# Kernel optimization log

Hardware: AMD Instinct MI355X
Metric: run time of the kernel (lower is better)

## Reference

```python
import jax, jax.numpy as jnp
import numpy as np

NUM_FEATURES = 602
NUM_CLASSES = 41
HIDDEN = 8
HEADS1 = 8
HEADS2 = 1
N_NODES = 100000
N_EDGES = 1600000
NEG_SLOPE = 0.2  # PyG GATConv default leaky_relu slope
EPS = 1e-16      # PyG softmax denominator epsilon


def gat_conv(x, edge_index, W, att_src, att_dst, bias, heads, out_ch, concat):
    """Faithful PyG GATConv forward (eval mode, dropout disabled).
    x: [N, F_in], edge_index: [2, E] with row0=src, row1=dst.
    W: [F_in, heads*out_ch], att_src/att_dst: [heads, out_ch], bias: [heads*out_ch] or [out_ch].
    """
    N = x.shape[0]
    h = (x @ W).reshape(N, heads, out_ch)              # [N, H, C]
    a_src = jnp.einsum('nhc,hc->nh', h, att_src)       # [N, H]
    a_dst = jnp.einsum('nhc,hc->nh', h, att_dst)       # [N, H]
    src, dst = edge_index[0], edge_index[1]
    e = jax.nn.leaky_relu(a_src[src] + a_dst[dst], NEG_SLOPE)  # [E, H]
    # segment softmax over incoming edges of each dst node
    m = jax.ops.segment_max(e, dst, num_segments=N)    # [N, H]
    e = jnp.exp(e - m[dst])
    denom = jax.ops.segment_sum(e, dst, num_segments=N)  # [N, H]
    alpha = e / (denom[dst] + EPS)                     # [E, H]
    msg = h[src] * alpha[:, :, None]                   # [E, H, C]
    out = jax.ops.segment_sum(msg, dst, num_segments=N)  # [N, H, C]
    if concat:
        out = out.reshape(N, heads * out_ch)
    else:
        out = out.mean(axis=1)
    return out + bias


def setup_inputs() -> dict:
    key = jax.random.key(0)
    ks = jax.random.split(key, 10)
    x = jax.random.normal(ks[0], (N_NODES, NUM_FEATURES), dtype=jnp.float32)
    edge_index = jax.random.randint(ks[1], (2, N_EDGES), 0, N_NODES, dtype=jnp.int64)
    s = 0.1
    W1 = jax.random.normal(ks[2], (NUM_FEATURES, HEADS1 * HIDDEN), dtype=jnp.float32) * s
    att_src1 = jax.random.normal(ks[3], (HEADS1, HIDDEN), dtype=jnp.float32) * s
    att_dst1 = jax.random.normal(ks[4], (HEADS1, HIDDEN), dtype=jnp.float32) * s
    b1 = jnp.zeros((HEADS1 * HIDDEN,), dtype=jnp.float32)
    W2 = jax.random.normal(ks[5], (HEADS1 * HIDDEN, HEADS2 * NUM_CLASSES), dtype=jnp.float32) * s
    att_src2 = jax.random.normal(ks[6], (HEADS2, NUM_CLASSES), dtype=jnp.float32) * s
    att_dst2 = jax.random.normal(ks[7], (HEADS2, NUM_CLASSES), dtype=jnp.float32) * s
    b2 = jnp.zeros((NUM_CLASSES,), dtype=jnp.float32)
    return {"x": x, "edge_index": edge_index, "W1": W1, "att_src1": att_src1,
            "att_dst1": att_dst1, "b1": b1, "W2": W2, "att_src2": att_src2,
            "att_dst2": att_dst2, "b2": b2}


def reference(x, edge_index, W1, att_src1, att_dst1, b1, W2, att_src2, att_dst2, b2):
    # eval mode: all F.dropout calls are identity
    h = gat_conv(x, edge_index, W1, att_src1, att_dst1, b1, HEADS1, HIDDEN, concat=True)
    h = jax.nn.elu(h)
    h = gat_conv(h, edge_index, W2, att_src2, att_dst2, b2, HEADS2, NUM_CLASSES, concat=False)
    return jax.nn.log_softmax(h, axis=1)
```

## Files before the change

kernel.cpp:

```cpp
#include <hip/hip_runtime.h>
#include <math.h>

#define NN 100000
#define NE 1600000
#define F_IN 602
#define H1 8
#define C1 8
#define F_MID 64
#define NC 41
#define H2_LD 48
#define NEG_SLOPE 0.2f
#define WT_LD 640

#define LRELU(x) fmaxf((x), NEG_SLOPE * (x))

typedef __attribute__((ext_vector_type(8))) short short8;
typedef __attribute__((ext_vector_type(4))) float f32x4;

__device__ inline unsigned short f2bf(float f) {
    unsigned u = __builtin_bit_cast(unsigned, f);
    unsigned r = (u + 0x7FFFu + ((u >> 16) & 1u)) >> 16;
    return (unsigned short)r;
}

__global__ void zero_kernel(int4* __restrict__ p, int n4)
{
    int i = blockIdx.x * blockDim.x + threadIdx.x;
    if (i < n4) p[i] = make_int4(0, 0, 0, 0);
}

__global__ void prep_wt_kernel(const float* __restrict__ W, unsigned short* __restrict__ Wt)
{
    int idx = blockIdx.x * blockDim.x + threadIdx.x;
    if (idx >= F_MID * WT_LD) return;
    int col = idx / WT_LD, k = idx % WT_LD;
    Wt[idx] = (k < F_IN) ? f2bf(W[k * F_MID + col]) : (unsigned short)0;
}

__global__ __launch_bounds__(256) void gemm1_mfma(
    const float* __restrict__ x, const unsigned short* __restrict__ Wt,
    float* __restrict__ h, int N)
{
    __shared__ unsigned short As[64][40];
    __shared__ unsigned short Bs[64][40];

    int t = threadIdx.x;
    int lane = t & 63;
    int w = t >> 6;
    int l16 = lane & 15, lg = lane >> 4;
    int n0 = blockIdx.x * 64;

    int arow = t >> 2, aseg = t & 3;
    int grow = n0 + arow;
    const float* xrow = x + (size_t)(grow < N ? grow : 0) * F_IN + aseg * 8;
    int bcol = t >> 2;
    const unsigned short* wrow = Wt + (size_t)bcol * WT_LD + aseg * 8;

    f32x4 acc[4] = {};
    float2 av[4];
    uint4  bv;

    #pragma unroll
    for (int i = 0; i < 4; ++i) av[i] = *(const float2*)(xrow + i * 2);
    bv = *(const uint4*)(wrow);

    for (int kt = 0; kt < 19; ++kt) {
        __syncthreads();
        {
            unsigned short tmp[8];
            #pragma unroll
            for (int i = 0; i < 4; ++i) {
                tmp[i * 2]     = f2bf(av[i].x);
                tmp[i * 2 + 1] = f2bf(av[i].y);
            }
            *(uint4*)(&As[arow][aseg * 8]) = *(uint4*)tmp;
            *(uint4*)(&Bs[bcol][aseg * 8]) = bv;
        }
        __syncthreads();

        if (kt < 18) {
            int k0 = (kt + 1) * 32;
            if (kt + 1 < 18) {
                #pragma unroll
                for (int i = 0; i < 4; ++i) av[i] = *(const float2*)(xrow + k0 + i * 2);
            } else {
                #pragma unroll
                for (int i = 0; i < 4; ++i) {
                    int k = k0 + aseg * 8 + i * 2;
                    float a = (k < F_IN)     ? xrow[k0 + i * 2]     : 0.f;
                    float b = (k + 1 < F_IN) ? xrow[k0 + i * 2 + 1] : 0.f;
                    av[i] = make_float2(a, b);
                }
            }
            bv = *(const uint4*)(wrow + k0);
        }

        short8 afrag = *(const short8*)(&As[w * 16 + l16][lg * 8]);
        short8 bfrag[4];
        #pragma unroll
        for (int n = 0; n < 4; ++n)
            bfrag[n] = *(const short8*)(&Bs[n * 16 + l16][lg * 8]);
        #pragma unroll
        for (int n = 0; n < 4; ++n)
            acc[n] = __builtin_amdgcn_mfma_f32_16x16x32_bf16(afrag, bfrag[n], acc[n], 0, 0, 0);
    }

    #pragma unroll
    for (int r = 0; r < 4; ++r) {
        int row = n0 + w * 16 + lg * 4 + r;
        if (row < N) {
            #pragma unroll
            for (int n = 0; n < 4; ++n)
                h[(size_t)row * F_MID + n * 16 + l16] = acc[n][r];
        }
    }
}

__global__ void attn1_kernel(const float* __restrict__ h,
                             const float* __restrict__ attS,
                             const float* __restrict__ attD,
                             float* __restrict__ asrc, float* __restrict__ adst, int N)
{
    int idx = blockIdx.x * blockDim.x + threadIdx.x;
    if (idx >= N * H1) return;
    int n = idx >> 3, hh = idx & 7;
    float s = 0.f, d = 0.f;
    #pragma unroll
    for (int c = 0; c < C1; ++c) {
        float v = h[n * F_MID + hh * C1 + c];
        s += v * attS[hh * C1 + c];
        d += v * attD[hh * C1 + c];
    }
    asrc[idx] = s;
    adst[idx] = d;
}

__global__ void deg_kernel(const int* __restrict__ dst, int* __restrict__ deg, int E)
{
    int e = blockIdx.x * blockDim.x + threadIdx.x;
    if (e < E) atomicAdd(&deg[dst[e]], 1);
}

__global__ void scan1_kernel(const int* __restrict__ deg, int* __restrict__ bsum, int N)
{
    int b = blockIdx.x, t = threadIdx.x;
    int base = b * 1024 + t * 16;
    int s = 0;
    #pragma unroll
    for (int i = 0; i < 16; ++i) { int idx = base + i; if (idx < N) s += deg[idx]; }
    #pragma unroll
    for (int o = 32; o > 0; o >>= 1) s += __shfl_down(s, o);
    if (t == 0) bsum[b] = s;
}

__global__ void scan2_kernel(const int* __restrict__ bsum, int* __restrict__ boff,
                             int nb, int* __restrict__ offs, int N, int E)
{
    __shared__ int buf[128];
    int t = threadIdx.x;
    int v = (t < nb) ? bsum[t] : 0;
    buf[t] = v;
    __syncthreads();
    for (int o = 1; o < 128; o <<= 1) {
        int u = (t >= o) ? buf[t - o] : 0;
        __syncthreads();
        buf[t] += u;
        __syncthreads();
    }
    if (t < nb) boff[t] = buf[t] - v;
    if (t == 0) offs[N] = E;
}

__global__ void scan3_kernel(const int* __restrict__ deg, const int* __restrict__ boff,
                             int* __restrict__ offs, int N)
{
    int b = blockIdx.x, t = threadIdx.x;
    int base = b * 1024 + t * 16;
    int loc[16];
    int s = 0;
    #pragma unroll
    for (int i = 0; i < 16; ++i) {
        int idx = base + i;
        loc[i] = (idx < N) ? deg[idx] : 0;
        s += loc[i];
    }
    int inc = s;
    #pragma unroll
    for (int o = 1; o < 64; o <<= 1) {
        int u = __shfl_up(inc, o);
        if (t >= o) inc += u;
    }
    int run = inc - s + boff[b];
    #pragma unroll
    for (int i = 0; i < 16; ++i) {
        int idx = base + i;
        if (idx < N) offs[idx] = run;
        run += loc[i];
    }
}

__global__ void scatter_kernel(const int* __restrict__ src, const int* __restrict__ dst,
                               const int* __restrict__ offs, int* __restrict__ cursor,
                               int* __restrict__ srcs, int E)
{
    int e = blockIdx.x * blockDim.x + threadIdx.x;
    if (e < E) {
        int d = dst[e];
        int pos = offs[d] + atomicAdd(&cursor[d], 1);
        srcs[pos] = src[e];
    }
}

__global__ void agg1_kernel(const int* __restrict__ offs, const int* __restrict__ srcs,
                            const float* __restrict__ h1,
                            const float* __restrict__ asrc, const float* __restrict__ adst,
                            const float* __restrict__ b1,
                            float* __restrict__ out1, int N)
{
    int wave = (blockIdx.x * blockDim.x + threadIdx.x) >> 6;
    int lane = threadIdx.x & 63;
    if (wave >= N) return;
    int n = wave;
    int hh = lane >> 3;
    int beg = offs[n], end = offs[n + 1];
    float ad = adst[n * H1 + hh];

    float m = -INFINITY, den = 0.f, acc = 0.f;
    int i = beg;
    for (; i + 8 <= end; i += 8) {
        int s[8];
        #pragma unroll
        for (int j = 0; j < 8; ++j) s[j] = srcs[i + j];
        float a[8], v[8];
        #pragma unroll
        for (int j = 0; j < 8; ++j) a[j] = asrc[s[j] * H1 + hh];
        #pragma unroll
        for (int j = 0; j < 8; ++j) v[j] = h1[s[j] * F_MID + lane];
        float e[8];
        #pragma unroll
        for (int j = 0; j < 8; ++j) e[j] = LRELU(a[j] + ad);
        float m8 = fmaxf(fmaxf(fmaxf(e[0], e[1]), fmaxf(e[2], e[3])),
                         fmaxf(fmaxf(e[4], e[5]), fmaxf(e[6], e[7])));
        float mn = fmaxf(m, m8);
        float sc = __expf(m - mn);
        float p[8];
        #pragma unroll
        for (int j = 0; j < 8; ++j) p[j] = __expf(e[j] - mn);
        den = den * sc + (((p[0] + p[1]) + (p[2] + p[3])) + ((p[4] + p[5]) + (p[6] + p[7])));
        acc = acc * sc + (((p[0] * v[0] + p[1] * v[1]) + (p[2] * v[2] + p[3] * v[3]))
                        + ((p[4] * v[4] + p[5] * v[5]) + (p[6] * v[6] + p[7] * v[7])));
        m = mn;
    }
    for (; i < end; ++i) {
        int s = srcs[i];
        float e = LRELU(asrc[s * H1 + hh] + ad);
        float hv = h1[s * F_MID + lane];
        float mn = fmaxf(m, e);
        float sc = __expf(m - mn);
        float p  = __expf(e - mn);
        den = den * sc + p;
        acc = acc * sc + p * hv;
        m = mn;
    }
    float inv = 1.f / (den + 1e-16f);
    float v = acc * inv + b1[lane];
    out1[n * F_MID + lane] = v > 0.f ? v : expm1f(v);
}

__global__ __launch_bounds__(256) void gemm2_kernel(
    const float* __restrict__ out1, const float* __restrict__ W2,
    float* __restrict__ h2p, int N)
{
    __shared__ float ws[F_MID * NC];
    for (int i = threadIdx.x; i < F_MID * NC; i += 256) ws[i] = W2[i];
    __syncthreads();
    int idx = blockIdx.x * blockDim.x + threadIdx.x;
    if (idx >= N * NC) return;
    int n = idx / NC, j = idx % NC;
    const float* row = out1 + n * F_MID;
    float acc = 0.f;
    #pragma unroll
    for (int k = 0; k < F_MID; ++k) acc += row[k] * ws[k * NC + j];
    h2p[n * H2_LD + j] = acc;
}

__global__ void attn2_kernel(float* __restrict__ h2p,
                             const float* __restrict__ attS,
                             const float* __restrict__ attD,
                             float* __restrict__ adst, int N)
{
    int n = blockIdx.x * blockDim.x + threadIdx.x;
    if (n >= N) return;
    float s = 0.f, d = 0.f;
    #pragma unroll
    for (int j = 0; j < NC; ++j) {
        float v = h2p[n * H2_LD + j];
        s += v * attS[j];
        d += v * attD[j];
    }
    h2p[n * H2_LD + NC] = s;
    adst[n] = d;
}

__global__ void agg2_kernel(const int* __restrict__ offs, const int* __restrict__ srcs,
                            const float* __restrict__ h2p,
                            const float* __restrict__ adst,
                            const float* __restrict__ b2,
                            float* __restrict__ out, int N)
{
    int wave = (blockIdx.x * blockDim.x + threadIdx.x) >> 6;
    int lane = threadIdx.x & 63;
    if (wave >= N) return;
    int n = wave;
    int beg = offs[n], end = offs[n + 1];
    float ad = adst[n];
    bool act = lane < NC;
    int li = act ? lane : NC;

    float m = -INFINITY, den = 0.f, acc = 0.f;
    int i = beg;
    for (; i + 8 <= end; i += 8) {
        int s[8];
        #pragma unroll
        for (int j = 0; j < 8; ++j) s[j] = srcs[i + j];
        float hv[8];
        #pragma unroll
        for (int j = 0; j < 8; ++j) hv[j] = h2p[s[j] * H2_LD + li];
        float a[8];
        #pragma unroll
        for (int j = 0; j < 8; ++j) a[j] = __shfl(hv[j], NC);
        float e[8];
        #pragma unroll
        for (int j = 0; j < 8; ++j) e[j] = LRELU(a[j] + ad);
        float m8 = fmaxf(fmaxf(fmaxf(e[0], e[1]), fmaxf(e[2], e[3])),
                         fmaxf(fmaxf(e[4], e[5]), fmaxf(e[6], e[7])));
        float mn = fmaxf(m, m8);
        float sc = __expf(m - mn);
        float p[8];
        #pragma unroll
        for (int j = 0; j < 8; ++j) p[j] = __expf(e[j] - mn);
        den = den * sc + (((p[0] + p[1]) + (p[2] + p[3])) + ((p[4] + p[5]) + (p[6] + p[7])));
        acc = acc * sc + (((p[0] * hv[0] + p[1] * hv[1]) + (p[2] * hv[2] + p[3] * hv[3]))
                        + ((p[4] * hv[4] + p[5] * hv[5]) + (p[6] * hv[6] + p[7] * hv[7])));
        m = mn;
    }
    for (; i < end; ++i) {
        int s = srcs[i];
        float hv = h2p[s * H2_LD + li];
        float a = __shfl(hv, NC);
        float e = LRELU(a + ad);
        float mn = fmaxf(m, e);
        float sc = __expf(m - mn);
        float p  = __expf(e - mn);
        den = den * sc + p;
        acc = acc * sc + p * hv;
        m = mn;
    }
    float inv = 1.f / (den + 1e-16f);
    float v = act ? acc * inv + b2[lane] : -INFINITY;
    float mm = v;
    #pragma unroll
    for (int o = 32; o > 0; o >>= 1) mm = fmaxf(mm, __shfl_xor(mm, o));
    float ex = act ? __expf(v - mm) : 0.f;
    float S = ex;
    #pragma unroll
    for (int o = 32; o > 0; o >>= 1) S += __shfl_xor(S, o);
    if (act) out[n * NC + lane] = v - mm - logf(S);
}

extern "C" void kernel_launch(void* const* d_in, const int* in_sizes, int n_in,
                              void* d_out, int out_size, void* d_ws, size_t ws_size,
                              hipStream_t stream)
{
    const float* x     = (const float*)d_in[0];
    const int*   ei    = (const int*)  d_in[1];
    const float* W1    = (const float*)d_in[2];
    const float* attS1 = (const float*)d_in[3];
    const float* attD1 = (const float*)d_in[4];
    const float* b1    = (const float*)d_in[5];
    const float* W2    = (const float*)d_in[6];
    const float* attS2 = (const float*)d_in[7];
    const float* attD2 = (const float*)d_in[8];
    const float* b2    = (const float*)d_in[9];
    float* out = (float*)d_out;

    const int N = NN, E = NE;
    const int* src = ei;
    const int* dst = ei + E;

    char* p = (char*)d_ws;
    auto alloc = [&](size_t bytes) { char* r = p; p += (bytes + 255) & ~255ull; return r; };
    float* h1    = (float*)alloc((size_t)N * F_MID * 4);
    float* asrc1 = (float*)alloc((size_t)N * H1 * 4);
    float* adst1 = (float*)alloc((size_t)N * H1 * 4);
    float* out1  = (float*)alloc((size_t)N * F_MID * 4);
    float* h2p   = (float*)alloc((size_t)N * H2_LD * 4);
    float* adst2 = (float*)alloc((size_t)N * 4);
    int*   deg   = (int*)alloc((size_t)2 * N * 4);
    int*   cursor= deg + N;
    int*   offs  = (int*)alloc((size_t)(N + 1) * 4);
    int*   srcs  = (int*)alloc((size_t)E * 4);
    unsigned short* Wt = (unsigned short*)alloc((size_t)F_MID * WT_LD * 2);
    const int NB = (N + 1023) / 1024;
    int*   bsum  = (int*)alloc((size_t)NB * 4);
    int*   boff  = (int*)alloc((size_t)NB * 4);

    const int n4 = (2 * N) / 4;
    zero_kernel<<<(n4 + 255) / 256, 256, 0, stream>>>((int4*)deg, n4);

    prep_wt_kernel<<<(F_MID * WT_LD + 255) / 256, 256, 0, stream>>>(W1, Wt);
    gemm1_mfma<<<(N + 63) / 64, 256, 0, stream>>>(x, Wt, h1, N);
    attn1_kernel<<<(N * H1 + 255) / 256, 256, 0, stream>>>(h1, attS1, attD1, asrc1, adst1, N);
    deg_kernel<<<(E + 255) / 256, 256, 0, stream>>>(dst, deg, E);
    scan1_kernel<<<NB, 64, 0, stream>>>(deg, bsum, N);
    scan2_kernel<<<1, 128, 0, stream>>>(bsum, boff, NB, offs, N, E);
    scan3_kernel<<<NB, 64, 0, stream>>>(deg, boff, offs, N);
    scatter_kernel<<<(E + 255) / 256, 256, 0, stream>>>(src, dst, offs, cursor, srcs, E);
    agg1_kernel<<<(N * 64 + 255) / 256, 256, 0, stream>>>(offs, srcs, h1, asrc1, adst1, b1, out1, N);
    gemm2_kernel<<<(N * NC + 255) / 256, 256, 0, stream>>>(out1, W2, h2p, N);
    attn2_kernel<<<(N + 255) / 256, 256, 0, stream>>>(h2p, attS2, attD2, adst2, N);
    agg2_kernel<<<(N * 64 + 255) / 256, 256, 0, stream>>>(offs, srcs, h2p, adst2, b2, out, N);
}
```

Measured before the change: 475.2 us.

## Fuse GAT pipeline stages into mega kernels with bf16 hidden features

```diff
diff --git a/kernel.cpp b/kernel.cpp
--- a/kernel.cpp
+++ b/kernel.cpp
@@ -11,6 +11,9 @@
 #define H2_LD 48
 #define NEG_SLOPE 0.2f
 #define WT_LD 640
+#define GB1 ((NN + 63) / 64)
+#define DGB 1024
+#define ATB ((NN * H1 + 255) / 256)
 
 #define LRELU(x) fmaxf((x), NEG_SLOPE * (x))
 
@@ -22,6 +25,10 @@
     unsigned r = (u + 0x7FFFu + ((u >> 16) & 1u)) >> 16;
     return (unsigned short)r;
 }
+__device__ inline float bf2f(unsigned short u) {
+    unsigned v = ((unsigned)u) << 16;
+    return __builtin_bit_cast(float, v);
+}
 
 __global__ void zero_kernel(int4* __restrict__ p, int n4)
 {
@@ -29,26 +36,50 @@
     if (i < n4) p[i] = make_int4(0, 0, 0, 0);
 }
 
-__global__ void prep_wt_kernel(const float* __restrict__ W, unsigned short* __restrict__ Wt)
+__global__ void prep_kernel(const float* __restrict__ W1, const float* __restrict__ W2,
+                            const float* __restrict__ attS2, const float* __restrict__ attD2,
+                            unsigned short* __restrict__ Wt,
+                            float* __restrict__ wsv, float* __restrict__ wdv)
 {
     int idx = blockIdx.x * blockDim.x + threadIdx.x;
-    if (idx >= F_MID * WT_LD) return;
-    int col = idx / WT_LD, k = idx % WT_LD;
-    Wt[idx] = (k < F_IN) ? f2bf(W[k * F_MID + col]) : (unsigned short)0;
-}
-
-__global__ __launch_bounds__(256) void gemm1_mfma(
+    if (idx < F_MID * WT_LD) {
+        int col = idx / WT_LD, k = idx % WT_LD;
+        Wt[idx] = (k < F_IN) ? f2bf(W1[k * F_MID + col]) : (unsigned short)0;
+    } else if (idx < F_MID * WT_LD + F_MID) {
+        int k = idx - F_MID * WT_LD;
+        float s = 0.f, d = 0.f;
+        #pragma unroll
+        for (int j = 0; j < NC; ++j) {
+            float w = W2[k * NC + j];
+            s += w * attS2[j];
+            d += w * attD2[j];
+        }
+        wsv[k] = s; wdv[k] = d;
+    }
+}
+
+__global__ __launch_bounds__(256) void mega1_kernel(
     const float* __restrict__ x, const unsigned short* __restrict__ Wt,
-    float* __restrict__ h, int N)
+    unsigned short* __restrict__ h1b,
+    const int* __restrict__ dst, int* __restrict__ deg, int* __restrict__ rank,
+    int N, int E)
 {
     __shared__ unsigned short As[64][40];
     __shared__ unsigned short Bs[64][40];
 
+    int bid = blockIdx.x;
     int t = threadIdx.x;
+
+    if (bid < DGB) {
+        for (int e = bid * 256 + t; e < E; e += DGB * 256)
+            rank[e] = atomicAdd(&deg[dst[e]], 1);
+        return;
+    }
+
     int lane = t & 63;
     int w = t >> 6;
     int l16 = lane & 15, lg = lane >> 4;
-    int n0 = blockIdx.x * 64;
+    int n0 = (bid - DGB) * 64;
 
     int arow = t >> 2, aseg = t & 3;
     int grow = n0 + arow;
@@ -111,34 +142,9 @@
         if (row < N) {
             #pragma unroll
             for (int n = 0; n < 4; ++n)
-                h[(size_t)row * F_MID + n * 16 + l16] = acc[n][r];
+                h1b[(size_t)row * F_MID + n * 16 + l16] = f2bf(acc[n][r]);
         }
     }
-}
-
-__global__ void attn1_kernel(const float* __restrict__ h,
-                             const float* __restrict__ attS,
-                             const float* __restrict__ attD,
-                             float* __restrict__ asrc, float* __restrict__ adst, int N)
-{
-    int idx = blockIdx.x * blockDim.x + threadIdx.x;
-    if (idx >= N * H1) return;
-    int n = idx >> 3, hh = idx & 7;
-    float s = 0.f, d = 0.f;
-    #pragma unroll
-    for (int c = 0; c < C1; ++c) {
-        float v = h[n * F_MID + hh * C1 + c];
-        s += v * attS[hh * C1 + c];
-        d += v * attD[hh * C1 + c];
-    }
-    asrc[idx] = s;
-    adst[idx] = d;
-}
-
-__global__ void deg_kernel(const int* __restrict__ dst, int* __restrict__ deg, int E)
-{
-    int e = blockIdx.x * blockDim.x + threadIdx.x;
-    if (e < E) atomicAdd(&deg[dst[e]], 1);
 }
 
 __global__ void scan1_kernel(const int* __restrict__ deg, int* __restrict__ bsum, int N)
@@ -199,26 +205,51 @@
     }
 }
 
-__global__ void scatter_kernel(const int* __restrict__ src, const int* __restrict__ dst,
-                               const int* __restrict__ offs, int* __restrict__ cursor,
-                               int* __restrict__ srcs, int E)
-{
-    int e = blockIdx.x * blockDim.x + threadIdx.x;
-    if (e < E) {
-        int d = dst[e];
-        int pos = offs[d] + atomicAdd(&cursor[d], 1);
-        srcs[pos] = src[e];
-    }
-}
-
-__global__ void agg1_kernel(const int* __restrict__ offs, const int* __restrict__ srcs,
-                            const float* __restrict__ h1,
-                            const float* __restrict__ asrc, const float* __restrict__ adst,
-                            const float* __restrict__ b1,
-                            float* __restrict__ out1, int N)
-{
-    int wave = (blockIdx.x * blockDim.x + threadIdx.x) >> 6;
-    int lane = threadIdx.x & 63;
+__global__ void mega2_kernel(
+    const unsigned short* __restrict__ h1b,
+    const float* __restrict__ attS, const float* __restrict__ attD,
+    float* __restrict__ asrc, float* __restrict__ adst,
+    const int* __restrict__ src, const int* __restrict__ dst,
+    const int* __restrict__ rank, const int* __restrict__ offs,
+    int* __restrict__ srcs, int N, int E)
+{
+    int bid = blockIdx.x, t = threadIdx.x;
+    if (bid < DGB) {
+        for (int e = bid * 256 + t; e < E; e += DGB * 256)
+            srcs[offs[dst[e]] + rank[e]] = src[e];
+        return;
+    }
+    int idx = (bid - DGB) * 256 + t;
+    if (idx >= N * H1) return;
+    int n = idx >> 3, hh = idx & 7;
+    float s = 0.f, d = 0.f;
+    #pragma unroll
+    for (int c = 0; c < C1; ++c) {
+        float v = bf2f(h1b[n * F_MID + hh * C1 + c]);
+        s += v * attS[hh * C1 + c];
+        d += v * attD[hh * C1 + c];
+    }
+    asrc[idx] = s;
+    adst[idx] = d;
+}
+
+__global__ __launch_bounds__(256) void agg1_kernel(
+    const int* __restrict__ offs, const int* __restrict__ srcs,
+    const unsigned short* __restrict__ h1b,
+    const float* __restrict__ asrc, const float* __restrict__ adst,
+    const float* __restrict__ b1, const float* __restrict__ W2,
+    const float* __restrict__ wsv, const float* __restrict__ wdv,
+    float* __restrict__ h2p, float* __restrict__ adst2, int N)
+{
+    __shared__ float Ws[F_MID][NC];
+    __shared__ float wsv_s[F_MID], wdv_s[F_MID];
+    int t = threadIdx.x;
+    for (int i = t; i < F_MID * NC; i += 256) Ws[i / NC][i % NC] = W2[i];
+    if (t < F_MID) { wsv_s[t] = wsv[t]; wdv_s[t] = wdv[t]; }
+    __syncthreads();
+
+    int wave = (blockIdx.x * 256 + t) >> 6;
+    int lane = t & 63;
     if (wave >= N) return;
     int n = wave;
     int hh = lane >> 3;
@@ -235,7 +266,7 @@
         #pragma unroll
         for (int j = 0; j < 8; ++j) a[j] = asrc[s[j] * H1 + hh];
         #pragma unroll
-        for (int j = 0; j < 8; ++j) v[j] = h1[s[j] * F_MID + lane];
+        for (int j = 0; j < 8; ++j) v[j] = bf2f(h1b[(size_t)s[j] * F_MID + lane]);
         float e[8];
         #pragma unroll
         for (int j = 0; j < 8; ++j) e[j] = LRELU(a[j] + ad);
@@ -254,7 +285,7 @@
     for (; i < end; ++i) {
         int s = srcs[i];
         float e = LRELU(asrc[s * H1 + hh] + ad);
-        float hv = h1[s * F_MID + lane];
+        float hv = bf2f(h1b[(size_t)s * F_MID + lane]);
         float mn = fmaxf(m, e);
         float sc = __expf(m - mn);
         float p  = __expf(e - mn);
@@ -263,43 +294,21 @@
         m = mn;
     }
     float inv = 1.f / (den + 1e-16f);
-    float v = acc * inv + b1[lane];
-    out1[n * F_MID + lane] = v > 0.f ? v : expm1f(v);
-}
-
-__global__ __launch_bounds__(256) void gemm2_kernel(
-    const float* __restrict__ out1, const float* __restrict__ W2,
-    float* __restrict__ h2p, int N)
-{
-    __shared__ float ws[F_MID * NC];
-    for (int i = threadIdx.x; i < F_MID * NC; i += 256) ws[i] = W2[i];
-    __syncthreads();
-    int idx = blockIdx.x * blockDim.x + threadIdx.x;
-    if (idx >= N * NC) return;
-    int n = idx / NC, j = idx % NC;
-    const float* row = out1 + n * F_MID;
-    float acc = 0.f;
-    #pragma unroll
-    for (int k = 0; k < F_MID; ++k) acc += row[k] * ws[k * NC + j];
-    h2p[n * H2_LD + j] = acc;
-}
-
-__global__ void attn2_kernel(float* __restrict__ h2p,
-                             const float* __restrict__ attS,
-                             const float* __restrict__ attD,
-                             float* __restrict__ adst, int N)
-{
-    int n = blockIdx.x * blockDim.x + threadIdx.x;
-    if (n >= N) return;
-    float s = 0.f, d = 0.f;
-    #pragma unroll
-    for (int j = 0; j < NC; ++j) {
-        float v = h2p[n * H2_LD + j];
-        s += v * attS[j];
-        d += v * attD[j];
-    }
-    h2p[n * H2_LD + NC] = s;
-    adst[n] = d;
+    float o = acc * inv + b1[lane];
+    o = o > 0.f ? o : expm1f(o);
+
+    int jl = lane < NC ? lane : 0;
+    float hj = 0.f, sd = 0.f, dd = 0.f;
+    #pragma unroll
+    for (int k = 0; k < F_MID; ++k) {
+        float bv = __shfl(o, k);
+        hj = fmaf(bv, Ws[k][jl], hj);
+        sd = fmaf(bv, wsv_s[k], sd);
+        dd = fmaf(bv, wdv_s[k], dd);
+    }
+    if (lane < NC)       h2p[(size_t)n * H2_LD + lane] = hj;
+    else if (lane == NC) h2p[(size_t)n * H2_LD + NC]   = sd;
+    if (lane == 0)       adst2[n] = dd;
 }
 
 __global__ void agg2_kernel(const int* __restrict__ offs, const int* __restrict__ srcs,
@@ -325,7 +334,7 @@
         for (int j = 0; j < 8; ++j) s[j] = srcs[i + j];
         float hv[8];
         #pragma unroll
-        for (int j = 0; j < 8; ++j) hv[j] = h2p[s[j] * H2_LD + li];
+        for (int j = 0; j < 8; ++j) hv[j] = h2p[(size_t)s[j] * H2_LD + li];
         float a[8];
         #pragma unroll
         for (int j = 0; j < 8; ++j) a[j] = __shfl(hv[j], NC);
@@ -346,7 +355,7 @@
     }
     for (; i < end; ++i) {
         int s = srcs[i];
-        float hv = h2p[s * H2_LD + li];
+        float hv = h2p[(size_t)s * H2_LD + li];
         float a = __shfl(hv, NC);
         float e = LRELU(a + ad);
         float mn = fmaxf(m, e);
@@ -390,34 +399,32 @@
 
     char* p = (char*)d_ws;
     auto alloc = [&](size_t bytes) { char* r = p; p += (bytes + 255) & ~255ull; return r; };
-    float* h1    = (float*)alloc((size_t)N * F_MID * 4);
+    unsigned short* h1b = (unsigned short*)alloc((size_t)N * F_MID * 2);
     float* asrc1 = (float*)alloc((size_t)N * H1 * 4);
     float* adst1 = (float*)alloc((size_t)N * H1 * 4);
-    float* out1  = (float*)alloc((size_t)N * F_MID * 4);
     float* h2p   = (float*)alloc((size_t)N * H2_LD * 4);
     float* adst2 = (float*)alloc((size_t)N * 4);
-    int*   deg   = (int*)alloc((size_t)2 * N * 4);
-    int*   cursor= deg + N;
+    int*   deg   = (int*)alloc((size_t)N * 4);
+    int*   rank  = (int*)alloc((size_t)E * 4);
     int*   offs  = (int*)alloc((size_t)(N + 1) * 4);
     int*   srcs  = (int*)alloc((size_t)E * 4);
     unsigned short* Wt = (unsigned short*)alloc((size_t)F_MID * WT_LD * 2);
+    float* wsv   = (float*)alloc((size_t)F_MID * 4);
+    float* wdv   = (float*)alloc((size_t)F_MID * 4);
     const int NB = (N + 1023) / 1024;
     int*   bsum  = (int*)alloc((size_t)NB * 4);
     int*   boff  = (int*)alloc((size_t)NB * 4);
 
-    const int n4 = (2 * N) / 4;
-    zero_kernel<<<(n4 + 255) / 256, 256, 0, stream>>>((int4*)deg, n4);
-
-    prep_wt_kernel<<<(F_MID * WT_LD + 255) / 256, 256, 0, stream>>>(W1, Wt);
-    gemm1_mfma<<<(N + 63) / 64, 256, 0, stream>>>(x, Wt, h1, N);
-    attn1_kernel<<<(N * H1 + 255) / 256, 256, 0, stream>>>(h1, attS1, attD1, asrc1, adst1, N);
-    deg_kernel<<<(E + 255) / 256, 256, 0, stream>>>(dst, deg, E);
+    zero_kernel<<<(N / 4 + 255) / 256, 256, 0, stream>>>((int4*)deg, N / 4);
+    prep_kernel<<<(F_MID * WT_LD + F_MID + 255) / 256, 256, 0, stream>>>(
+        W1, W2, attS2, attD2, Wt, wsv, wdv);
+    mega1_kernel<<<DGB + GB1, 256, 0, stream>>>(x, Wt, h1b, dst, deg, rank, N, E);
     scan1_kernel<<<NB, 64, 0, stream>>>(deg, bsum, N);
     scan2_kernel<<<1, 128, 0, stream>>>(bsum, boff, NB, offs, N, E);
     scan3_kernel<<<NB, 64, 0, stream>>>(deg, boff, offs, N);
-    scatter_kernel<<<(E + 255) / 256, 256, 0, stream>>>(src, dst, offs, cursor, srcs, E);
-    agg1_kernel<<<(N * 64 + 255) / 256, 256, 0, stream>>>(offs, srcs, h1, asrc1, adst1, b1, out1, N);
-    gemm2_kernel<<<(N * NC + 255) / 256, 256, 0, stream>>>(out1, W2, h2p, N);
-    attn2_kernel<<<(N + 255) / 256, 256, 0, stream>>>(h2p, attS2, attD2, adst2, N);
+    mega2_kernel<<<DGB + ATB, 256, 0, stream>>>(
+        h1b, attS1, attD1, asrc1, adst1, src, dst, rank, offs, srcs, N, E);
+    agg1_kernel<<<(N * 64 + 255) / 256, 256, 0, stream>>>(
+        offs, srcs, h1b, asrc1, adst1, b1, W2, wsv, wdv, h2p, adst2, N);
     agg2_kernel<<<(N * 64 + 255) / 256, 256, 0, stream>>>(offs, srcs, h2p, adst2, b2, out, N);
 }
```

After: 652.4 us. +37.3%, slower.
